# Kernel tuning notes

Hardware: AMD Instinct MI355X
Metric: run time of the kernel (lower is better)

Reference implementation:

```python
import jax, jax.numpy as jnp
import numpy as np

TEMPERATURE = 0.07
EPS = 1e-8  # torch cosine_similarity clamps the norm product at eps


def setup_inputs() -> dict:
    key = jax.random.key(0)
    k1, k2 = jax.random.split(key)
    B, D = 8192, 256
    u = jax.random.normal(k1, (B, D), dtype=jnp.float32)
    v = jax.random.normal(k2, (B, D), dtype=jnp.float32)
    return {"u": u, "v": v}


def _cos_sim_matrix(a, b):
    # pairwise cosine similarity: (a . b) / max(|a||b|, eps)
    dots = a @ b.T                                   # [B, B]
    an = jnp.linalg.norm(a, axis=-1)                 # [B]
    bn = jnp.linalg.norm(b, axis=-1)                 # [B]
    denom = jnp.maximum(an[:, None] * bn[None, :], EPS)
    return dots / denom


def reference(u, v):
    B = u.shape[0]
    sim_uv = _cos_sim_matrix(u, v) / TEMPERATURE     # [B, B]
    sim_uu = _cos_sim_matrix(u, u) / TEMPERATURE     # [B, B]
    eye = jnp.eye(B, dtype=bool)
    pos_loss = jnp.diagonal(sim_uv)                  # [B]
    neg_inf = jnp.array(-jnp.inf, dtype=sim_uv.dtype)
    # off-diagonal entries of both matrices, concatenated per row (2B-2 valid each)
    negative_sim = jnp.concatenate(
        [jnp.where(eye, neg_inf, sim_uv), jnp.where(eye, neg_inf, sim_uu)], axis=1
    )                                                # [B, 2B]
    neg_loss = jax.nn.logsumexp(negative_sim, axis=-1)  # [B]
    return (-pos_loss + neg_loss).mean()
```

## Files before the change

### kernel.cpp

```cpp
#include <hip/hip_runtime.h>
#include <stdint.h>

#define NB 8192
#define ND 256
#define NW 16384
#define NBLK 512
#define NTILE 32
#define SQRT_L2E_INVT 4.5398164f
#define LN2F 0.69314718056f

typedef float floatx4 __attribute__((ext_vector_type(4)));
typedef int   intx8   __attribute__((ext_vector_type(8)));

__global__ __launch_bounds__(512) void prep_kernel(
    const float* __restrict__ u, const float* __restrict__ v,
    unsigned char* __restrict__ W, float* __restrict__ rowsum,
    int* __restrict__ cnt)
{
    if (blockIdx.x == 0 && threadIdx.x == 0) *cnt = 0;
    if (blockIdx.x < 16) rowsum[blockIdx.x * 512 + threadIdx.x] = 0.f;
    const int t    = threadIdx.x;
    const int row  = blockIdx.x * 8 + (t >> 6);
    const int lane = t & 63;
    const float* src = (row < NB) ? (v + (size_t)row * ND)
                                  : (u + (size_t)(row - NB) * ND);
    float4 x = ((const float4*)src)[lane];
    float ss = x.x * x.x + x.y * x.y + x.z * x.z + x.w * x.w;
#pragma unroll
    for (int off = 1; off < 64; off <<= 1) ss += __shfl_xor(ss, off, 64);
    const float sc = rsqrtf(ss) * SQRT_L2E_INVT;
    int p = __builtin_amdgcn_cvt_pk_fp8_f32(x.x * sc, x.y * sc, 0, false);
    p     = __builtin_amdgcn_cvt_pk_fp8_f32(x.z * sc, x.w * sc, p, true);
    ((int*)(W + (size_t)row * ND))[lane] = p;
}

__device__ __forceinline__ void load_btile(const unsigned char* __restrict__ W,
                                           int cb, int tcol, int quad,
                                           intx8 (&dst)[2][2]) {
#pragma unroll
    for (int nt = 0; nt < 2; nt++) {
        const unsigned char* bp = W + (size_t)(cb + nt * 16 + tcol) * ND + quad * 32;
#pragma unroll
        for (int ks = 0; ks < 2; ks++)
            dst[nt][ks] = *(const intx8*)(bp + ks * 128);
    }
}

__device__ __forceinline__ void tile_step(const intx8 (&af)[4][2],
        const intx8 (&bt)[2][2], int cb, int rw0, float (&rsum)[4][4],
        float* __restrict__ pos, int quad, int tcol) {
    floatx4 acc[4][2];
#pragma unroll
    for (int mt = 0; mt < 4; mt++)
#pragma unroll
        for (int nt = 0; nt < 2; nt++) acc[mt][nt] = (floatx4){0.f, 0.f, 0.f, 0.f};
#pragma unroll
    for (int ks = 0; ks < 2; ks++)
#pragma unroll
        for (int mt = 0; mt < 4; mt++)
#pragma unroll
            for (int nt = 0; nt < 2; nt++)
                acc[mt][nt] = __builtin_amdgcn_mfma_scale_f32_16x16x128_f8f6f4(
                    af[mt][ks], bt[nt][ks], acc[mt][nt],
                    0, 0,
                    0, 127,
                    0, 127);

    const bool uvt = (cb >= rw0 && cb < rw0 + 64);
    const bool uut = (cb >= rw0 + NB && cb < rw0 + NB + 64);
    if (!uvt && !uut) {
#pragma unroll
        for (int mt = 0; mt < 4; mt++)
#pragma unroll
            for (int nt = 0; nt < 2; nt++)
#pragma unroll
                for (int reg = 0; reg < 4; reg++)
                    rsum[mt][reg] += __builtin_amdgcn_exp2f(acc[mt][nt][reg]);
    } else {
#pragma unroll
        for (int mt = 0; mt < 4; mt++)
#pragma unroll
            for (int nt = 0; nt < 2; nt++) {
                const int gcol = cb + nt * 16 + tcol;
#pragma unroll
                for (int reg = 0; reg < 4; reg++) {
                    const int grow = rw0 + mt * 16 + quad * 4 + reg;
                    float sc = acc[mt][nt][reg];
                    bool diag = (gcol == (uvt ? grow : grow + NB));
                    if (uvt && diag) pos[grow] = sc;
                    rsum[mt][reg] += diag ? 0.f : __builtin_amdgcn_exp2f(sc);
                }
            }
    }
}

__global__ __launch_bounds__(256, 2) void dcl_main(
    const unsigned char* __restrict__ W,
    float* __restrict__ rowsum,
    float* __restrict__ pos,
    int* __restrict__ cnt,
    float* __restrict__ out)
{
    const int b    = blockIdx.x;
    const int tid  = threadIdx.x;
    const int wave = tid >> 6;
    const int lane = tid & 63;
    const int quad = lane >> 4;
    const int tcol = lane & 15;
    const int rw0 = (((b >> 3) << 1) | (wave >> 1)) * 64;
    const int cw0 = (((b & 7) << 1) | (wave & 1)) * 1024;

    const unsigned char* Au = W + (size_t)NB * ND;

    intx8 af[4][2];
#pragma unroll
    for (int mt = 0; mt < 4; mt++) {
        const unsigned char* ap = Au + (size_t)(rw0 + mt * 16 + tcol) * ND + quad * 32;
#pragma unroll
        for (int ks = 0; ks < 2; ks++)
            af[mt][ks] = *(const intx8*)(ap + ks * 128);
    }

    float rsum[4][4];
#pragma unroll
    for (int mt = 0; mt < 4; mt++)
#pragma unroll
        for (int reg = 0; reg < 4; reg++) rsum[mt][reg] = 0.f;

    intx8 b0[2][2], b1[2][2];
    load_btile(W, cw0, tcol, quad, b0);
    for (int ct = 0; ct < NTILE; ct += 2) {
        const int cb = cw0 + ct * 32;
        load_btile(W, cb + 32, tcol, quad, b1);
        tile_step(af, b0, cb, rw0, rsum, pos, quad, tcol);
        if (ct + 2 < NTILE) load_btile(W, cb + 64, tcol, quad, b0);
        tile_step(af, b1, cb + 32, rw0, rsum, pos, quad, tcol);
    }

#pragma unroll
    for (int mt = 0; mt < 4; mt++)
#pragma unroll
        for (int reg = 0; reg < 4; reg++) {
            float vsum = rsum[mt][reg];
            vsum += __shfl_xor(vsum, 1, 64);
            vsum += __shfl_xor(vsum, 2, 64);
            vsum += __shfl_xor(vsum, 4, 64);
            vsum += __shfl_xor(vsum, 8, 64);
            if (tcol == 0)
                atomicAdd(&rowsum[rw0 + mt * 16 + quad * 4 + reg], vsum);
        }

    __threadfence();
    __syncthreads();
    __shared__ int amlast;
    if (tid == 0) amlast = (atomicAdd(cnt, 1) == NBLK - 1);
    __syncthreads();
    if (!amlast) return;
    __threadfence();

    float sacc = 0.f;
    for (int i = tid; i < NB; i += 256)
        sacc += logf(rowsum[i]) - pos[i] * LN2F;
#pragma unroll
    for (int off = 1; off < 64; off <<= 1) sacc += __shfl_xor(sacc, off, 64);
    __shared__ float wsum[4];
    if (lane == 0) wsum[wave] = sacc;
    __syncthreads();
    if (tid == 0)
        out[0] = (wsum[0] + wsum[1] + wsum[2] + wsum[3]) / (float)NB;
}

extern "C" void kernel_launch(void* const* d_in, const int* in_sizes, int n_in,
                              void* d_out, int out_size, void* d_ws, size_t ws_size,
                              hipStream_t stream) {
    const float* u = (const float*)d_in[0];
    const float* v = (const float*)d_in[1];
    float* out = (float*)d_out;

    char* ws = (char*)d_ws;
    unsigned char* W = (unsigned char*)ws;
    float* rowsum = (float*)(ws + (size_t)NW * ND);
    float* pos    = rowsum + NB;
    int*   cnt    = (int*)(pos + NB);

    prep_kernel<<<NW / 8, 512, 0, stream>>>(u, v, W, rowsum, cnt);
    dcl_main<<<NBLK, 256, 0, stream>>>(W, rowsum, pos, cnt, out);
}
```

Measured before the change: 167.1 us.

## Store fp8 operands in MFMA fragment order and triple-buffer B tiles

The prep kernel now writes the normalized fp8 matrix in a pre-swizzled layout of 16-row tiles, so that each lane's MFMA fragment is a contiguous 32-byte chunk. Global loads in the main kernel become fully coalesced across the wave instead of strided row reads. The column loop is also reworked into a fully unrolled schedule with three register buffers, issuing loads two tiles ahead. This raises register pressure, which could affect the two-blocks-per-CU occupancy target.

Measured after the change: 138.6 us. 17.1% less time.

```diff
diff --git a/kernel.cpp b/kernel.cpp
--- a/kernel.cpp
+++ b/kernel.cpp
@@ -12,9 +12,10 @@
 typedef float floatx4 __attribute__((ext_vector_type(4)));
 typedef int   intx8   __attribute__((ext_vector_type(8)));
 
+
 __global__ __launch_bounds__(512) void prep_kernel(
     const float* __restrict__ u, const float* __restrict__ v,
-    unsigned char* __restrict__ W, float* __restrict__ rowsum,
+    unsigned char* __restrict__ Wf, float* __restrict__ rowsum,
     int* __restrict__ cnt)
 {
     if (blockIdx.x == 0 && threadIdx.x == 0) *cnt = 0;
@@ -31,19 +32,17 @@
     const float sc = rsqrtf(ss) * SQRT_L2E_INVT;
     int p = __builtin_amdgcn_cvt_pk_fp8_f32(x.x * sc, x.y * sc, 0, false);
     p     = __builtin_amdgcn_cvt_pk_fp8_f32(x.z * sc, x.w * sc, p, true);
-    ((int*)(W + (size_t)row * ND))[lane] = p;
+    const int tile = row >> 4, r = row & 15, kc = lane >> 3;
+    ((int*)(Wf + (size_t)tile * 4096 + (kc * 16 + r) * 32))[lane & 7] = p;
 }
 
-__device__ __forceinline__ void load_btile(const unsigned char* __restrict__ W,
-                                           int cb, int tcol, int quad,
-                                           intx8 (&dst)[2][2]) {
-#pragma unroll
-    for (int nt = 0; nt < 2; nt++) {
-        const unsigned char* bp = W + (size_t)(cb + nt * 16 + tcol) * ND + quad * 32;
-#pragma unroll
-        for (int ks = 0; ks < 2; ks++)
-            dst[nt][ks] = *(const intx8*)(bp + ks * 128);
-    }
+__device__ __forceinline__ void load_btile(const unsigned char* __restrict__ Wf,
+                                           int cb, int lane, intx8 (&dst)[2][2]) {
+    const unsigned char* p = Wf + (size_t)(cb >> 4) * 4096 + lane * 32;
+    dst[0][0] = *(const intx8*)(p);
+    dst[0][1] = *(const intx8*)(p + 2048);
+    dst[1][0] = *(const intx8*)(p + 4096);
+    dst[1][1] = *(const intx8*)(p + 6144);
 }
 
 __device__ __forceinline__ void tile_step(const intx8 (&af)[4][2],
@@ -95,7 +94,7 @@
 }
 
 __global__ __launch_bounds__(256, 2) void dcl_main(
-    const unsigned char* __restrict__ W,
+    const unsigned char* __restrict__ Wf,
     float* __restrict__ rowsum,
     float* __restrict__ pos,
     int* __restrict__ cnt,
@@ -110,15 +109,13 @@
     const int rw0 = (((b >> 3) << 1) | (wave >> 1)) * 64;
     const int cw0 = (((b & 7) << 1) | (wave & 1)) * 1024;
 
-    const unsigned char* Au = W + (size_t)NB * ND;
-
     intx8 af[4][2];
 #pragma unroll
     for (int mt = 0; mt < 4; mt++) {
-        const unsigned char* ap = Au + (size_t)(rw0 + mt * 16 + tcol) * ND + quad * 32;
-#pragma unroll
-        for (int ks = 0; ks < 2; ks++)
-            af[mt][ks] = *(const intx8*)(ap + ks * 128);
+        const unsigned char* ap =
+            Wf + (size_t)(512 + ((rw0 + mt * 16) >> 4)) * 4096 + lane * 32;
+        af[mt][0] = *(const intx8*)(ap);
+        af[mt][1] = *(const intx8*)(ap + 2048);
     }
 
     float rsum[4][4];
@@ -127,15 +124,21 @@
 #pragma unroll
         for (int reg = 0; reg < 4; reg++) rsum[mt][reg] = 0.f;
 
-    intx8 b0[2][2], b1[2][2];
-    load_btile(W, cw0, tcol, quad, b0);
-    for (int ct = 0; ct < NTILE; ct += 2) {
-        const int cb = cw0 + ct * 32;
-        load_btile(W, cb + 32, tcol, quad, b1);
+    intx8 b0[2][2], b1[2][2], b2[2][2];
+    load_btile(Wf, cw0,      lane, b0);
+    load_btile(Wf, cw0 + 32, lane, b1);
+#pragma unroll
+    for (int g = 0; g < 10; g++) {
+        const int cb = cw0 + g * 96;
+        load_btile(Wf, cb + 64, lane, b2);
         tile_step(af, b0, cb, rw0, rsum, pos, quad, tcol);
-        if (ct + 2 < NTILE) load_btile(W, cb + 64, tcol, quad, b0);
+        load_btile(Wf, cb + 96, lane, b0);
         tile_step(af, b1, cb + 32, rw0, rsum, pos, quad, tcol);
+        load_btile(Wf, cb + 128, lane, b1);
+        tile_step(af, b2, cb + 64, rw0, rsum, pos, quad, tcol);
     }
+    tile_step(af, b0, cw0 + 30 * 32, rw0, rsum, pos, quad, tcol);
+    tile_step(af, b1, cw0 + 31 * 32, rw0, rsum, pos, quad, tcol);
 
 #pragma unroll
     for (int mt = 0; mt < 4; mt++)
@@ -178,11 +181,11 @@
     float* out = (float*)d_out;
 
     char* ws = (char*)d_ws;
-    unsigned char* W = (unsigned char*)ws;
+    unsigned char* Wf = (unsigned char*)ws;
     float* rowsum = (float*)(ws + (size_t)NW * ND);
     float* pos    = rowsum + NB;
     int*   cnt    = (int*)(pos + NB);
 
-    prep_kernel<<<NW / 8, 512, 0, stream>>>(u, v, W, rowsum, cnt);
-    dcl_main<<<NBLK, 256, 0, stream>>>(W, rowsum, pos, cnt, out);
+    prep_kernel<<<NW / 8, 512, 0, stream>>>(u, v, Wf, rowsum, cnt);
+    dcl_main<<<NBLK, 256, 0, stream>>>(Wf, rowsum, pos, cnt, out);
 }
```
